# Optimization experiments

Measured on AMD Instinct MI355X. Metric: run time of the kernel, lower is better.

The kernel has to match this reference:

```python
import jax, jax.numpy as jnp
import numpy as np

D_MODEL = 1024
D_INNER = 2048   # d_model * expansion_factor(2)
D_CONV = 4
N_EXPERTS = 8
TOP_K = 2


def setup_inputs() -> dict:
    key = jax.random.key(0)
    ks = jax.random.split(key, 6)
    s = 0.02
    return {
        "x": jax.random.normal(ks[0], (4, 2048, D_MODEL), jnp.float32),
        "Wr": jax.random.normal(ks[1], (N_EXPERTS, D_MODEL), jnp.float32) * s,
        "br": jnp.zeros((N_EXPERTS,), jnp.float32),
        "Win": jax.random.normal(ks[2], (N_EXPERTS, 2 * D_INNER, D_MODEL), jnp.float32) * s,
        "conv_w": jax.random.normal(ks[3], (N_EXPERTS, D_INNER, D_CONV), jnp.float32) * s,
        "conv_b": jnp.zeros((N_EXPERTS, D_INNER), jnp.float32),
        "Dp": jnp.ones((N_EXPERTS, D_INNER), jnp.float32),
        "Wout": jax.random.normal(ks[4], (N_EXPERTS, D_MODEL, D_INNER), jnp.float32) * s,
    }


def reference(x, Wr, br, Win, conv_w, conv_b, Dp, Wout):
    B, L, C = x.shape
    xf = x.reshape(-1, C)                                   # [N, C]
    logits = xf @ Wr.T + br                                 # [N, E]
    probs = jax.nn.softmax(logits.astype(jnp.float32), axis=-1)
    tw, ti = jax.lax.top_k(probs, TOP_K)                    # [N, k]
    tw = tw / jnp.sum(tw, axis=-1, keepdims=True)
    oh = jax.nn.one_hot(ti, N_EXPERTS, dtype=jnp.float32)   # [N, k, E]
    load = oh.sum(1).mean(0)                                # [E]
    aux_loss = jnp.sum(load * load)
    # per-token combine weight for each expert (sum over top-k slots)
    cw = jnp.einsum('nk,nke->ne', tw, oh)                   # [N, E]
    out = jnp.zeros_like(xf)
    for j in range(N_EXPERTS):
        # Per-token expert (L=1 inside the original loop): causal depthwise
        # conv with left padding reduces to last-tap * x + bias.
        xz = xf @ Win[j].T                                  # [N, 2*D_INNER]
        xi, z = xz[:, :D_INNER], xz[:, D_INNER:]
        xa = jax.nn.silu(xi * conv_w[j, :, -1] + conv_b[j])
        y = xa * Dp[j] * jax.nn.silu(z)
        out = out + cw[:, j:j + 1].astype(xf.dtype) * (y @ Wout[j].T)
    return out.reshape(B, L, C), aux_loss
```

## Files before the change

kernel.cpp:

```cpp
#include <hip/hip_runtime.h>
#include <hip/hip_bf16.h>
#include <stdint.h>

#define NTOK 8192
#define CDIM 1024
#define DIN  2048
#define NEXP 8
#define NSLOT (NTOK * 2)

typedef __bf16 bf16x8 __attribute__((ext_vector_type(8)));
typedef float  f32x4  __attribute__((ext_vector_type(4)));

typedef __attribute__((address_space(1))) const unsigned char GBUF;
typedef __attribute__((address_space(3))) unsigned char LBUF;

__device__ __forceinline__ void gload_lds16(const void* g, void* l) {
    __builtin_amdgcn_global_load_lds((GBUF*)g, (LBUF*)l, 16, 0, 0);
}

__device__ __forceinline__ ushort f2bf(float f) {
    union { float f; unsigned u; } v; v.f = f;
    unsigned u = v.u;
    u += 0x7fffu + ((u >> 16) & 1u);
    return (ushort)(u >> 16);
}
__device__ __forceinline__ float bf2f(ushort u) {
    union { float f; unsigned u; } v; v.u = ((unsigned)u) << 16; return v.f;
}
__device__ __forceinline__ float silu_f(float x) { return x / (1.f + __expf(-x)); }

__device__ __forceinline__ bf16x8 lds_swz(const ushort* L, int row, int kof) {
    return *(const bf16x8*)&L[row * 64 + ((((kof >> 3) ^ row) & 7) << 3)];
}

__global__ void __launch_bounds__(256) k_cvt(const float* __restrict__ src,
                                             ushort* __restrict__ dst, int n4) {
    int i = blockIdx.x * 256 + threadIdx.x;
    int stride = gridDim.x * 256;
    for (; i < n4; i += stride) {
        float4 v = ((const float4*)src)[i];
        ushort4 o;
        o.x = f2bf(v.x); o.y = f2bf(v.y); o.z = f2bf(v.z); o.w = f2bf(v.w);
        ((ushort4*)dst)[i] = o;
    }
}

__global__ void __launch_bounds__(256) k_router(
    const float* __restrict__ x, const float* __restrict__ Wr,
    const float* __restrict__ br, int* __restrict__ counts,
    int* __restrict__ tok_e, float* __restrict__ tok_w,
    ushort* __restrict__ xb) {
    int wave = blockIdx.x * 4 + (threadIdx.x >> 6);
    int lane = threadIdx.x & 63;
    const float4* row = (const float4*)(x + (size_t)wave * CDIM);
    ushort4* xrow = (ushort4*)(xb + (size_t)wave * CDIM);
    float acc[NEXP];
#pragma unroll
    for (int e = 0; e < NEXP; ++e) acc[e] = 0.f;
#pragma unroll
    for (int j = 0; j < 4; ++j) {
        float4 v = row[j * 64 + lane];
        ushort4 o;
        o.x = f2bf(v.x); o.y = f2bf(v.y); o.z = f2bf(v.z); o.w = f2bf(v.w);
        xrow[j * 64 + lane] = o;
#pragma unroll
        for (int e = 0; e < NEXP; ++e) {
            float4 w = ((const float4*)(Wr + e * CDIM))[j * 64 + lane];
            acc[e] += v.x * w.x + v.y * w.y + v.z * w.z + v.w * w.w;
        }
    }
#pragma unroll
    for (int off = 32; off > 0; off >>= 1)
#pragma unroll
        for (int e = 0; e < NEXP; ++e) acc[e] += __shfl_xor(acc[e], off, 64);
    if (lane == 0) {
        float l[NEXP];
#pragma unroll
        for (int e = 0; e < NEXP; ++e) l[e] = acc[e] + br[e];
        int i0 = 0; float l0 = l[0];
#pragma unroll
        for (int e = 1; e < NEXP; ++e) if (l[e] > l0) { l0 = l[e]; i0 = e; }
        int i1 = -1; float l1 = -1e30f;
#pragma unroll
        for (int e = 0; e < NEXP; ++e) if (e != i0 && l[e] > l1) { l1 = l[e]; i1 = e; }
        float s  = __expf(l1 - l0);
        float w0 = 1.f / (1.f + s);
        float w1 = 1.f - w0;
        tok_e[wave * 2] = i0; tok_e[wave * 2 + 1] = i1;
        tok_w[wave * 2] = w0; tok_w[wave * 2 + 1] = w1;
        atomicAdd(&counts[i0], 1); atomicAdd(&counts[i1], 1);
    }
}

__global__ void k_scan(const int* __restrict__ counts, int* __restrict__ offsets,
                       float* __restrict__ out_aux) {
    if (threadIdx.x == 0 && blockIdx.x == 0) {
        int o = 0;
        for (int e = 0; e < NEXP; ++e) { offsets[e] = o; o += counts[e]; }
        offsets[NEXP] = o;
        float aux = 0.f;
        for (int e = 0; e < NEXP; ++e) {
            float ld = (float)counts[e] * (1.f / (float)NTOK);
            aux += ld * ld;
        }
        *out_aux = aux;
    }
}

__global__ void __launch_bounds__(256) k_scatter(
    const int* __restrict__ tok_e, const float* __restrict__ tok_w,
    const int* __restrict__ offsets, int* __restrict__ cursor,
    int* __restrict__ perm_token, int* __restrict__ tok_slot) {
    int t = blockIdx.x * 256 + threadIdx.x;
    if (t >= NTOK) return;
#pragma unroll
    for (int k = 0; k < 2; ++k) {
        int e = tok_e[t * 2 + k];
        int pos = atomicAdd(&cursor[e], 1);
        int s = offsets[e] + pos;
        perm_token[s] = t;
        tok_slot[t * 2 + k] = s;
    }
}

__global__ void __launch_bounds__(512, 2) k_gemm1(
    const ushort* __restrict__ xb, const ushort* __restrict__ Winb,
    const float* __restrict__ conv_w, const float* __restrict__ conv_b,
    const float* __restrict__ Dp, const int* __restrict__ counts,
    const int* __restrict__ offsets, const int* __restrict__ perm_token,
    ushort* __restrict__ y) {
    int h = blockIdx.x;
    int vb = (h & 7) * 160 + (h >> 3);
    int e   = vb / 160;
    int r   = vb % 160;
    int mt0 = r >> 4;
    int nt  = r & 15;
    int cnt = counts[e];
    if (cnt == 0) return;
    int base = offsets[e];
    int mtiles = (cnt + 255) >> 8;
    int n0 = nt * 128;

    __shared__ ushort aL[2][256 * 64];
    __shared__ ushort bL[2][256 * 64];

    int tid = threadIdx.x, lane = tid & 63, w = tid >> 6;
    int Mw = w >> 1, Nw = w & 1;
    const ushort* WinE = Winb + (size_t)e * (2 * DIN) * CDIM;
    int schunk = ((tid & 7) ^ ((tid >> 3) & 7)) << 3;

    uint bsrc[4];
#pragma unroll
    for (int i = 0; i < 4; ++i) {
        int rr = i * 64 + (tid >> 3);
        int grow = (rr < 128) ? (n0 + rr) : (DIN + n0 + (rr - 128));
        bsrc[i] = (uint)grow * CDIM + schunk;
    }

#define STAGE1(bi, kk0) do { \
        gload_lds16(xb   + asrc[0] + (kk0), &aL[bi][(0 * 512 + tid) * 8]); \
        gload_lds16(xb   + asrc[1] + (kk0), &aL[bi][(1 * 512 + tid) * 8]); \
        gload_lds16(xb   + asrc[2] + (kk0), &aL[bi][(2 * 512 + tid) * 8]); \
        gload_lds16(xb   + asrc[3] + (kk0), &aL[bi][(3 * 512 + tid) * 8]); \
        gload_lds16(WinE + bsrc[0] + (kk0), &bL[bi][(0 * 512 + tid) * 8]); \
        gload_lds16(WinE + bsrc[1] + (kk0), &bL[bi][(1 * 512 + tid) * 8]); \
        gload_lds16(WinE + bsrc[2] + (kk0), &bL[bi][(2 * 512 + tid) * 8]); \
        gload_lds16(WinE + bsrc[3] + (kk0), &bL[bi][(3 * 512 + tid) * 8]); \
    } while (0)

    for (int mt = mt0; mt < mtiles; mt += 10) {
        int rem = cnt - mt * 256;
        uint asrc[4];
#pragma unroll
        for (int i = 0; i < 4; ++i) {
            int rr = i * 64 + (tid >> 3);
            int sidx = base + mt * 256 + (rr < rem ? rr : 0);
            asrc[i] = (uint)perm_token[sidx] * CDIM + schunk;
        }

        f32x4 accXi[4][4], accZ[4][4];
#pragma unroll
        for (int m = 0; m < 4; ++m)
#pragma unroll
            for (int n = 0; n < 4; ++n) {
                accXi[m][n] = f32x4{0.f, 0.f, 0.f, 0.f};
                accZ[m][n]  = f32x4{0.f, 0.f, 0.f, 0.f};
            }

        STAGE1(0, 0);
        __syncthreads();
#pragma unroll 2
        for (int kt = 0; kt < 16; ++kt) {
            int cur = kt & 1;
            if (kt < 15) STAGE1(cur ^ 1, (kt + 1) * 64);
            const ushort* A = &aL[cur][0];
            const ushort* B = &bL[cur][0];
#pragma unroll
            for (int kk = 0; kk < 64; kk += 32) {
                int kof = kk + (lane >> 4) * 8;
                bf16x8 af[4], bxi[4], bz[4];
#pragma unroll
                for (int m = 0; m < 4; ++m)
                    af[m] = lds_swz(A, Mw * 64 + m * 16 + (lane & 15), kof);
#pragma unroll
                for (int n = 0; n < 4; ++n) {
                    int cl = Nw * 64 + n * 16 + (lane & 15);
                    bxi[n] = lds_swz(B, cl, kof);
                    bz[n]  = lds_swz(B, 128 + cl, kof);
                }
#pragma unroll
                for (int m = 0; m < 4; ++m)
#pragma unroll
                    for (int n = 0; n < 4; ++n) {
                        accXi[m][n] = __builtin_amdgcn_mfma_f32_16x16x32_bf16(af[m], bxi[n], accXi[m][n], 0, 0, 0);
                        accZ[m][n]  = __builtin_amdgcn_mfma_f32_16x16x32_bf16(af[m], bz[n],  accZ[m][n],  0, 0, 0);
                    }
            }
            __syncthreads();
        }
#pragma unroll
        for (int n = 0; n < 4; ++n) {
            int c = n0 + Nw * 64 + n * 16 + (lane & 15);
            float cwl = conv_w[((size_t)e * DIN + c) * 4 + 3];
            float cb  = conv_b[(size_t)e * DIN + c];
            float dp  = Dp[(size_t)e * DIN + c];
#pragma unroll
            for (int m = 0; m < 4; ++m)
#pragma unroll
                for (int q = 0; q < 4; ++q) {
                    int rl = Mw * 64 + m * 16 + (lane >> 4) * 4 + q;
                    if (rl < rem) {
                        int slot = base + mt * 256 + rl;
                        float xi = accXi[m][n][q], z = accZ[m][n][q];
                        float yv = silu_f(xi * cwl + cb) * dp * silu_f(z);
                        y[(size_t)slot * DIN + c] = f2bf(yv);
                    }
                }
        }
    }
#undef STAGE1
}

__global__ void __launch_bounds__(512, 2) k_gemm2(
    const ushort* __restrict__ y, const ushort* __restrict__ Woutb,
    const int* __restrict__ counts, const int* __restrict__ offsets,
    ushort* __restrict__ so) {
    int h = blockIdx.x;
    int vb = (h & 7) * 32 + (h >> 3);
    int e   = vb >> 5;
    int r   = vb & 31;
    int nt  = r >> 3;
    int sp  = r & 7;
    int cnt = counts[e];
    if (cnt == 0) return;
    int base = offsets[e];
    int mtiles = (cnt + 255) >> 8;
    int c0 = nt * 256;

    __shared__ ushort aL[2][256 * 64];
    __shared__ ushort bL[2][256 * 64];

    int tid = threadIdx.x, lane = tid & 63, w = tid >> 6;
    int Mw = w >> 2, Nw = w & 3;
    const ushort* WoutE = Woutb + (size_t)e * CDIM * DIN;
    int schunk = ((tid & 7) ^ ((tid >> 3) & 7)) << 3;

    uint bsrc[4];
#pragma unroll
    for (int i = 0; i < 4; ++i) {
        int rr = i * 64 + (tid >> 3);
        bsrc[i] = (uint)(c0 + rr) * DIN + schunk;
    }

#define STAGE2(bi, kk0) do { \
        gload_lds16(y     + asrc[0] + (kk0), &aL[bi][(0 * 512 + tid) * 8]); \
        gload_lds16(y     + asrc[1] + (kk0), &aL[bi][(1 * 512 + tid) * 8]); \
        gload_lds16(y     + asrc[2] + (kk0), &aL[bi][(2 * 512 + tid) * 8]); \
        gload_lds16(y     + asrc[3] + (kk0), &aL[bi][(3 * 512 + tid) * 8]); \
        gload_lds16(WoutE + bsrc[0] + (kk0), &bL[bi][(0 * 512 + tid) * 8]); \
        gload_lds16(WoutE + bsrc[1] + (kk0), &bL[bi][(1 * 512 + tid) * 8]); \
        gload_lds16(WoutE + bsrc[2] + (kk0), &bL[bi][(2 * 512 + tid) * 8]); \
        gload_lds16(WoutE + bsrc[3] + (kk0), &bL[bi][(3 * 512 + tid) * 8]); \
    } while (0)

    for (int mt = sp; mt < mtiles; mt += 8) {
        int rem = cnt - mt * 256;
        uint asrc[4];
#pragma unroll
        for (int i = 0; i < 4; ++i) {
            int rr = i * 64 + (tid >> 3);
            int slot = base + mt * 256 + (rr < rem ? rr : 0);
            asrc[i] = (uint)slot * DIN + schunk;
        }
        f32x4 acc[8][4];
#pragma unroll
        for (int m = 0; m < 8; ++m)
#pragma unroll
            for (int n = 0; n < 4; ++n) acc[m][n] = f32x4{0.f, 0.f, 0.f, 0.f};

        STAGE2(0, 0);
        __syncthreads();
#pragma unroll 2
        for (int kt = 0; kt < 32; ++kt) {
            int cur = kt & 1;
            if (kt < 31) STAGE2(cur ^ 1, (kt + 1) * 64);
            const ushort* A = &aL[cur][0];
            const ushort* B = &bL[cur][0];
#pragma unroll
            for (int kk = 0; kk < 64; kk += 32) {
                int kof = kk + (lane >> 4) * 8;
                bf16x8 af[8], bfr[4];
#pragma unroll
                for (int m = 0; m < 8; ++m)
                    af[m] = lds_swz(A, Mw * 128 + m * 16 + (lane & 15), kof);
#pragma unroll
                for (int n = 0; n < 4; ++n)
                    bfr[n] = lds_swz(B, Nw * 64 + n * 16 + (lane & 15), kof);
#pragma unroll
                for (int m = 0; m < 8; ++m)
#pragma unroll
                    for (int n = 0; n < 4; ++n)
                        acc[m][n] = __builtin_amdgcn_mfma_f32_16x16x32_bf16(af[m], bfr[n], acc[m][n], 0, 0, 0);
            }
            __syncthreads();
        }
#pragma unroll
        for (int m = 0; m < 8; ++m)
#pragma unroll
            for (int q = 0; q < 4; ++q) {
                int rl = Mw * 128 + m * 16 + (lane >> 4) * 4 + q;
                if (rl < rem) {
                    int slot = base + mt * 256 + rl;
#pragma unroll
                    for (int n = 0; n < 4; ++n) {
                        int col = c0 + Nw * 64 + n * 16 + (lane & 15);
                        so[(size_t)slot * CDIM + col] = f2bf(acc[m][n][q]);
                    }
                }
            }
    }
#undef STAGE2
}

__global__ void __launch_bounds__(256) k_combine(
    const ushort* __restrict__ so, const int* __restrict__ tok_slot,
    const float* __restrict__ tok_w, float* __restrict__ out) {
    int i = blockIdx.x * 256 + threadIdx.x;
    int t  = i >> 7;
    int c8 = (i & 127) << 3;
    int s0 = tok_slot[t * 2], s1 = tok_slot[t * 2 + 1];
    float w0 = tok_w[t * 2],  w1 = tok_w[t * 2 + 1];
    uint4 a = *(const uint4*)(so + (size_t)s0 * CDIM + c8);
    uint4 b = *(const uint4*)(so + (size_t)s1 * CDIM + c8);
    const ushort* au = (const ushort*)&a;
    const ushort* bu = (const ushort*)&b;
    float4 o0, o1;
    o0.x = w0 * bf2f(au[0]) + w1 * bf2f(bu[0]);
    o0.y = w0 * bf2f(au[1]) + w1 * bf2f(bu[1]);
    o0.z = w0 * bf2f(au[2]) + w1 * bf2f(bu[2]);
    o0.w = w0 * bf2f(au[3]) + w1 * bf2f(bu[3]);
    o1.x = w0 * bf2f(au[4]) + w1 * bf2f(bu[4]);
    o1.y = w0 * bf2f(au[5]) + w1 * bf2f(bu[5]);
    o1.z = w0 * bf2f(au[6]) + w1 * bf2f(bu[6]);
    o1.w = w0 * bf2f(au[7]) + w1 * bf2f(bu[7]);
    float4* dst = (float4*)(out + (size_t)t * CDIM + c8);
    dst[0] = o0; dst[1] = o1;
}

extern "C" void kernel_launch(void* const* d_in, const int* in_sizes, int n_in,
                              void* d_out, int out_size, void* d_ws, size_t ws_size,
                              hipStream_t stream) {
    const float* x      = (const float*)d_in[0];
    const float* Wr     = (const float*)d_in[1];
    const float* br     = (const float*)d_in[2];
    const float* Win    = (const float*)d_in[3];
    const float* conv_w = (const float*)d_in[4];
    const float* conv_b = (const float*)d_in[5];
    const float* Dp     = (const float*)d_in[6];
    const float* Wout   = (const float*)d_in[7];
    float* out = (float*)d_out;

    char* ws = (char*)d_ws;
    int*    counts     = (int*)(ws + 0);
    int*    offsets    = (int*)(ws + 64);
    int*    cursor     = (int*)(ws + 128);
    int*    tok_e      = (int*)(ws + 4096);
    float*  tok_w      = (float*)(ws + 4096 + 1 * 65536);
    int*    perm_token = (int*)(ws + 4096 + 2 * 65536);
    int*    tok_slot   = (int*)(ws + 4096 + 3 * 65536);
    const size_t MB = 1u << 20;
    ushort* y     = (ushort*)(ws + MB);
    ushort* xb    = (ushort*)(ws + MB + 67108864);
    ushort* winb  = (ushort*)(ws + MB + 67108864 + 16777216);
    ushort* woutb = (ushort*)(ws + MB + 67108864 + 16777216 + 67108864);
    ushort* so    = winb;

    hipMemsetAsync(ws, 0, 256, stream);

    k_cvt<<<2048, 256, 0, stream>>>(Win,  winb,  NEXP * 2 * DIN * CDIM / 4);
    k_cvt<<<1024, 256, 0, stream>>>(Wout, woutb, NEXP * CDIM * DIN / 4);

    k_router<<<NTOK / 4, 256, 0, stream>>>(x, Wr, br, counts, tok_e, tok_w, xb);
    k_scan<<<1, 64, 0, stream>>>(counts, offsets, out + (size_t)NTOK * CDIM);
    k_scatter<<<NTOK / 256, 256, 0, stream>>>(tok_e, tok_w, offsets, cursor, perm_token, tok_slot);

    k_gemm1<<<NEXP * 160, 512, 0, stream>>>(xb, winb, conv_w, conv_b, Dp,
                                            counts, offsets, perm_token, y);
    k_gemm2<<<NEXP * 32, 512, 0, stream>>>(y, woutb, counts, offsets, so);
    k_combine<<<NTOK * 128 / 256, 256, 0, stream>>>(so, tok_slot, tok_w, out);
}
```

Measured before the change: 632.2 us.

## Use 4-stage K=32 LDS pipeline with vmcnt waits in both expert GEMMs

Replaces the double-buffered K=64 tiles with a four-slot ring of K=32 tiles in both expert GEMMs. Each step waits on outstanding global-to-LDS loads with explicit s_waitcnt vmcnt and a bare s_barrier instead of __syncthreads, so three tiles stay in flight. The MFMA sections are wrapped in s_setprio, and the XOR swizzle is dropped for a plain 32-wide row layout. The aim is to hide global load latency better; the cost is possible LDS bank conflicts from the unswizzled 64-byte rows and more barriers per unit of K.

```diff
diff --git a/kernel.cpp b/kernel.cpp
--- a/kernel.cpp
+++ b/kernel.cpp
@@ -29,9 +29,8 @@
 }
 __device__ __forceinline__ float silu_f(float x) { return x / (1.f + __expf(-x)); }
 
-__device__ __forceinline__ bf16x8 lds_swz(const ushort* L, int row, int kof) {
-    return *(const bf16x8*)&L[row * 64 + ((((kof >> 3) ^ row) & 7) << 3)];
-}
+#define WAITV(N) asm volatile("s_waitcnt vmcnt(" #N ")" ::: "memory")
+#define BARR     __builtin_amdgcn_s_barrier()
 
 __global__ void __launch_bounds__(256) k_cvt(const float* __restrict__ src,
                                              ushort* __restrict__ dst, int n4) {
@@ -141,42 +140,24 @@
     int mtiles = (cnt + 255) >> 8;
     int n0 = nt * 128;
 
-    __shared__ ushort aL[2][256 * 64];
-    __shared__ ushort bL[2][256 * 64];
+    __shared__ ushort aL[4][256 * 32];
+    __shared__ ushort bL[4][256 * 32];
 
     int tid = threadIdx.x, lane = tid & 63, w = tid >> 6;
     int Mw = w >> 1, Nw = w & 1;
     const ushort* WinE = Winb + (size_t)e * (2 * DIN) * CDIM;
-    int schunk = ((tid & 7) ^ ((tid >> 3) & 7)) << 3;
-
-    uint bsrc[4];
-#pragma unroll
-    for (int i = 0; i < 4; ++i) {
-        int rr = i * 64 + (tid >> 3);
-        int grow = (rr < 128) ? (n0 + rr) : (DIN + n0 + (rr - 128));
-        bsrc[i] = (uint)grow * CDIM + schunk;
-    }
-
-#define STAGE1(bi, kk0) do { \
-        gload_lds16(xb   + asrc[0] + (kk0), &aL[bi][(0 * 512 + tid) * 8]); \
-        gload_lds16(xb   + asrc[1] + (kk0), &aL[bi][(1 * 512 + tid) * 8]); \
-        gload_lds16(xb   + asrc[2] + (kk0), &aL[bi][(2 * 512 + tid) * 8]); \
-        gload_lds16(xb   + asrc[3] + (kk0), &aL[bi][(3 * 512 + tid) * 8]); \
-        gload_lds16(WinE + bsrc[0] + (kk0), &bL[bi][(0 * 512 + tid) * 8]); \
-        gload_lds16(WinE + bsrc[1] + (kk0), &bL[bi][(1 * 512 + tid) * 8]); \
-        gload_lds16(WinE + bsrc[2] + (kk0), &bL[bi][(2 * 512 + tid) * 8]); \
-        gload_lds16(WinE + bsrc[3] + (kk0), &bL[bi][(3 * 512 + tid) * 8]); \
-    } while (0)
+
+    int srow0 = w * 16 + (lane >> 2);
+    int srow1 = srow0 + 128;
+    int skc   = (lane & 3) * 8;
+
+    uint b0 = (uint)(n0 + srow0) * CDIM + skc;
+    uint b1 = (uint)(DIN + n0 + (srow1 - 128)) * CDIM + skc;
 
     for (int mt = mt0; mt < mtiles; mt += 10) {
         int rem = cnt - mt * 256;
-        uint asrc[4];
-#pragma unroll
-        for (int i = 0; i < 4; ++i) {
-            int rr = i * 64 + (tid >> 3);
-            int sidx = base + mt * 256 + (rr < rem ? rr : 0);
-            asrc[i] = (uint)perm_token[sidx] * CDIM + schunk;
-        }
+        uint a0 = (uint)perm_token[base + mt * 256 + (srow0 < rem ? srow0 : 0)] * CDIM + skc;
+        uint a1 = (uint)perm_token[base + mt * 256 + (srow1 < rem ? srow1 : 0)] * CDIM + skc;
 
         f32x4 accXi[4][4], accZ[4][4];
 #pragma unroll
@@ -187,37 +168,52 @@
                 accZ[m][n]  = f32x4{0.f, 0.f, 0.f, 0.f};
             }
 
-        STAGE1(0, 0);
-        __syncthreads();
-#pragma unroll 2
-        for (int kt = 0; kt < 16; ++kt) {
-            int cur = kt & 1;
-            if (kt < 15) STAGE1(cur ^ 1, (kt + 1) * 64);
-            const ushort* A = &aL[cur][0];
-            const ushort* B = &bL[cur][0];
-#pragma unroll
-            for (int kk = 0; kk < 64; kk += 32) {
-                int kof = kk + (lane >> 4) * 8;
-                bf16x8 af[4], bxi[4], bz[4];
-#pragma unroll
-                for (int m = 0; m < 4; ++m)
-                    af[m] = lds_swz(A, Mw * 64 + m * 16 + (lane & 15), kof);
+        auto stage = [&](int slot, int c) {
+            int ko = c * 32;
+            gload_lds16(xb   + a0 + ko, &aL[slot][w * 512]);
+            gload_lds16(xb   + a1 + ko, &aL[slot][(w + 8) * 512]);
+            gload_lds16(WinE + b0 + ko, &bL[slot][w * 512]);
+            gload_lds16(WinE + b1 + ko, &bL[slot][(w + 8) * 512]);
+        };
+        auto compute = [&](int slot) {
+            const ushort* A = aL[slot];
+            const ushort* B = bL[slot];
+            int ko = (lane >> 4) * 8;
+            bf16x8 af[4], bxi[4], bz[4];
+#pragma unroll
+            for (int m = 0; m < 4; ++m)
+                af[m] = *(const bf16x8*)&A[(Mw * 64 + m * 16 + (lane & 15)) * 32 + ko];
+#pragma unroll
+            for (int n = 0; n < 4; ++n) {
+                int cl = Nw * 64 + n * 16 + (lane & 15);
+                bxi[n] = *(const bf16x8*)&B[cl * 32 + ko];
+                bz[n]  = *(const bf16x8*)&B[(128 + cl) * 32 + ko];
+            }
+            __builtin_amdgcn_s_setprio(1);
+#pragma unroll
+            for (int m = 0; m < 4; ++m)
 #pragma unroll
                 for (int n = 0; n < 4; ++n) {
-                    int cl = Nw * 64 + n * 16 + (lane & 15);
-                    bxi[n] = lds_swz(B, cl, kof);
-                    bz[n]  = lds_swz(B, 128 + cl, kof);
+                    accXi[m][n] = __builtin_amdgcn_mfma_f32_16x16x32_bf16(af[m], bxi[n], accXi[m][n], 0, 0, 0);
+                    accZ[m][n]  = __builtin_amdgcn_mfma_f32_16x16x32_bf16(af[m], bz[n],  accZ[m][n],  0, 0, 0);
                 }
-#pragma unroll
-                for (int m = 0; m < 4; ++m)
-#pragma unroll
-                    for (int n = 0; n < 4; ++n) {
-                        accXi[m][n] = __builtin_amdgcn_mfma_f32_16x16x32_bf16(af[m], bxi[n], accXi[m][n], 0, 0, 0);
-                        accZ[m][n]  = __builtin_amdgcn_mfma_f32_16x16x32_bf16(af[m], bz[n],  accZ[m][n],  0, 0, 0);
-                    }
-            }
-            __syncthreads();
+            __builtin_amdgcn_s_setprio(0);
+        };
+
+        stage(0, 0); stage(1, 1); stage(2, 2);
+#pragma unroll 1
+        for (int c = 0; c < 28; c += 4) {
+            WAITV(8); BARR; stage(3, c + 3); compute(0);
+            WAITV(8); BARR; stage(0, c + 4); compute(1);
+            WAITV(8); BARR; stage(1, c + 5); compute(2);
+            WAITV(8); BARR; stage(2, c + 6); compute(3);
         }
+        WAITV(8); BARR; stage(3, 31); compute(0);
+        WAITV(8); BARR; compute(1);
+        WAITV(4); BARR; compute(2);
+        WAITV(0); BARR; compute(3);
+        BARR;
+
 #pragma unroll
         for (int n = 0; n < 4; ++n) {
             int c = n0 + Nw * 64 + n * 16 + (lane & 15);
@@ -238,7 +234,6 @@
                 }
         }
     }
-#undef STAGE1
 }
 
 __global__ void __launch_bounds__(512, 2) k_gemm2(
@@ -257,73 +252,72 @@
     int mtiles = (cnt + 255) >> 8;
     int c0 = nt * 256;
 
-    __shared__ ushort aL[2][256 * 64];
-    __shared__ ushort bL[2][256 * 64];
+    __shared__ ushort aL[4][256 * 32];
+    __shared__ ushort bL[4][256 * 32];
 
     int tid = threadIdx.x, lane = tid & 63, w = tid >> 6;
     int Mw = w >> 2, Nw = w & 3;
     const ushort* WoutE = Woutb + (size_t)e * CDIM * DIN;
-    int schunk = ((tid & 7) ^ ((tid >> 3) & 7)) << 3;
-
-    uint bsrc[4];
-#pragma unroll
-    for (int i = 0; i < 4; ++i) {
-        int rr = i * 64 + (tid >> 3);
-        bsrc[i] = (uint)(c0 + rr) * DIN + schunk;
-    }
-
-#define STAGE2(bi, kk0) do { \
-        gload_lds16(y     + asrc[0] + (kk0), &aL[bi][(0 * 512 + tid) * 8]); \
-        gload_lds16(y     + asrc[1] + (kk0), &aL[bi][(1 * 512 + tid) * 8]); \
-        gload_lds16(y     + asrc[2] + (kk0), &aL[bi][(2 * 512 + tid) * 8]); \
-        gload_lds16(y     + asrc[3] + (kk0), &aL[bi][(3 * 512 + tid) * 8]); \
-        gload_lds16(WoutE + bsrc[0] + (kk0), &bL[bi][(0 * 512 + tid) * 8]); \
-        gload_lds16(WoutE + bsrc[1] + (kk0), &bL[bi][(1 * 512 + tid) * 8]); \
-        gload_lds16(WoutE + bsrc[2] + (kk0), &bL[bi][(2 * 512 + tid) * 8]); \
-        gload_lds16(WoutE + bsrc[3] + (kk0), &bL[bi][(3 * 512 + tid) * 8]); \
-    } while (0)
+
+    int srow0 = w * 16 + (lane >> 2);
+    int srow1 = srow0 + 128;
+    int skc   = (lane & 3) * 8;
+
+    uint b0 = (uint)(c0 + srow0) * DIN + skc;
+    uint b1 = (uint)(c0 + srow1) * DIN + skc;
 
     for (int mt = sp; mt < mtiles; mt += 8) {
         int rem = cnt - mt * 256;
-        uint asrc[4];
-#pragma unroll
-        for (int i = 0; i < 4; ++i) {
-            int rr = i * 64 + (tid >> 3);
-            int slot = base + mt * 256 + (rr < rem ? rr : 0);
-            asrc[i] = (uint)slot * DIN + schunk;
+        uint a0 = (uint)(base + mt * 256 + (srow0 < rem ? srow0 : 0)) * DIN + skc;
+        uint a1 = (uint)(base + mt * 256 + (srow1 < rem ? srow1 : 0)) * DIN + skc;
+
+        f32x4 acc[8][4];
+#pragma unroll
+        for (int m = 0; m < 8; ++m)
+#pragma unroll
+            for (int n = 0; n < 4; ++n) acc[m][n] = f32x4{0.f, 0.f, 0.f, 0.f};
+
+        auto stage = [&](int slot, int c) {
+            int ko = c * 32;
+            gload_lds16(y     + a0 + ko, &aL[slot][w * 512]);
+            gload_lds16(y     + a1 + ko, &aL[slot][(w + 8) * 512]);
+            gload_lds16(WoutE + b0 + ko, &bL[slot][w * 512]);
+            gload_lds16(WoutE + b1 + ko, &bL[slot][(w + 8) * 512]);
+        };
+        auto compute = [&](int slot) {
+            const ushort* A = aL[slot];
+            const ushort* B = bL[slot];
+            int ko = (lane >> 4) * 8;
+            bf16x8 af[8], bfr[4];
+#pragma unroll
+            for (int m = 0; m < 8; ++m)
+                af[m] = *(const bf16x8*)&A[(Mw * 128 + m * 16 + (lane & 15)) * 32 + ko];
+#pragma unroll
+            for (int n = 0; n < 4; ++n)
+                bfr[n] = *(const bf16x8*)&B[(Nw * 64 + n * 16 + (lane & 15)) * 32 + ko];
+            __builtin_amdgcn_s_setprio(1);
+#pragma unroll
+            for (int m = 0; m < 8; ++m)
+#pragma unroll
+                for (int n = 0; n < 4; ++n)
+                    acc[m][n] = __builtin_amdgcn_mfma_f32_16x16x32_bf16(af[m], bfr[n], acc[m][n], 0, 0, 0);
+            __builtin_amdgcn_s_setprio(0);
+        };
+
+        stage(0, 0); stage(1, 1); stage(2, 2);
+#pragma unroll 1
+        for (int c = 0; c < 60; c += 4) {
+            WAITV(8); BARR; stage(3, c + 3); compute(0);
+            WAITV(8); BARR; stage(0, c + 4); compute(1);
+            WAITV(8); BARR; stage(1, c + 5); compute(2);
+            WAITV(8); BARR; stage(2, c + 6); compute(3);
         }
-        f32x4 acc[8][4];
-#pragma unroll
-        for (int m = 0; m < 8; ++m)
-#pragma unroll
-            for (int n = 0; n < 4; ++n) acc[m][n] = f32x4{0.f, 0.f, 0.f, 0.f};
-
-        STAGE2(0, 0);
-        __syncthreads();
-#pragma unroll 2
-        for (int kt = 0; kt < 32; ++kt) {
-            int cur = kt & 1;
-            if (kt < 31) STAGE2(cur ^ 1, (kt + 1) * 64);
-            const ushort* A = &aL[cur][0];
-            const ushort* B = &bL[cur][0];
-#pragma unroll
-            for (int kk = 0; kk < 64; kk += 32) {
-                int kof = kk + (lane >> 4) * 8;
-                bf16x8 af[8], bfr[4];
-#pragma unroll
-                for (int m = 0; m < 8; ++m)
-                    af[m] = lds_swz(A, Mw * 128 + m * 16 + (lane & 15), kof);
-#pragma unroll
-                for (int n = 0; n < 4; ++n)
-                    bfr[n] = lds_swz(B, Nw * 64 + n * 16 + (lane & 15), kof);
-#pragma unroll
-                for (int m = 0; m < 8; ++m)
-#pragma unroll
-                    for (int n = 0; n < 4; ++n)
-                        acc[m][n] = __builtin_amdgcn_mfma_f32_16x16x32_bf16(af[m], bfr[n], acc[m][n], 0, 0, 0);
-            }
-            __syncthreads();
-        }
+        WAITV(8); BARR; stage(3, 63); compute(0);
+        WAITV(8); BARR; compute(1);
+        WAITV(4); BARR; compute(2);
+        WAITV(0); BARR; compute(3);
+        BARR;
+
 #pragma unroll
         for (int m = 0; m < 8; ++m)
 #pragma unroll
@@ -339,7 +333,6 @@
                 }
             }
     }
-#undef STAGE2
 }
 
 __global__ void __launch_bounds__(256) k_combine(
```

After: 694.8 us. 1.1x slower.

## Interleave split prefetch with MFMA phases and raise wave priority in both GEMMs

Applied to the files above, without the earlier changes.

The k-loop of both expert GEMM kernels becomes four phases per k-tile. Each phase loads a subset of fragments from LDS, issues a quarter of the next tile's global-to-LDS copies, then runs its MFMA block with wave priority raised. Explicit vmcnt waits and raw barriers replace whole-tile staging plus __syncthreads, so copies overlap compute more finely and stalls shrink. The cost is more barriers per tile, fragile hand-counted waitcnt ordering, and loops no longer unrolled.

```diff
diff --git a/kernel.cpp b/kernel.cpp
--- a/kernel.cpp
+++ b/kernel.cpp
@@ -32,6 +32,9 @@
 __device__ __forceinline__ bf16x8 lds_swz(const ushort* L, int row, int kof) {
     return *(const bf16x8*)&L[row * 64 + ((((kof >> 3) ^ row) & 7) << 3)];
 }
+
+#define WAITV(N) asm volatile("s_waitcnt vmcnt(" #N ")" ::: "memory")
+#define BARR     __builtin_amdgcn_s_barrier()
 
 __global__ void __launch_bounds__(256) k_cvt(const float* __restrict__ src,
                                              ushort* __restrict__ dst, int n4) {
@@ -157,17 +160,6 @@
         bsrc[i] = (uint)grow * CDIM + schunk;
     }
 
-#define STAGE1(bi, kk0) do { \
-        gload_lds16(xb   + asrc[0] + (kk0), &aL[bi][(0 * 512 + tid) * 8]); \
-        gload_lds16(xb   + asrc[1] + (kk0), &aL[bi][(1 * 512 + tid) * 8]); \
-        gload_lds16(xb   + asrc[2] + (kk0), &aL[bi][(2 * 512 + tid) * 8]); \
-        gload_lds16(xb   + asrc[3] + (kk0), &aL[bi][(3 * 512 + tid) * 8]); \
-        gload_lds16(WinE + bsrc[0] + (kk0), &bL[bi][(0 * 512 + tid) * 8]); \
-        gload_lds16(WinE + bsrc[1] + (kk0), &bL[bi][(1 * 512 + tid) * 8]); \
-        gload_lds16(WinE + bsrc[2] + (kk0), &bL[bi][(2 * 512 + tid) * 8]); \
-        gload_lds16(WinE + bsrc[3] + (kk0), &bL[bi][(3 * 512 + tid) * 8]); \
-    } while (0)
-
     for (int mt = mt0; mt < mtiles; mt += 10) {
         int rem = cnt - mt * 256;
         uint asrc[4];
@@ -187,37 +179,84 @@
                 accZ[m][n]  = f32x4{0.f, 0.f, 0.f, 0.f};
             }
 
-        STAGE1(0, 0);
+        auto stgA = [&](int bi, int ko, int i, int j) {
+            gload_lds16(xb + asrc[i] + ko, &aL[bi][(i * 512 + tid) * 8]);
+            gload_lds16(xb + asrc[j] + ko, &aL[bi][(j * 512 + tid) * 8]);
+        };
+        auto stgB = [&](int bi, int ko, int i, int j) {
+            gload_lds16(WinE + bsrc[i] + ko, &bL[bi][(i * 512 + tid) * 8]);
+            gload_lds16(WinE + bsrc[j] + ko, &bL[bi][(j * 512 + tid) * 8]);
+        };
+
+        bf16x8 af0[4], af1[4], bx[4], bz[4];
+        stgA(0, 0, 0, 1); stgA(0, 0, 2, 3); stgB(0, 0, 0, 1); stgB(0, 0, 2, 3);
+
+#pragma unroll 1
+        for (int kt = 0; kt < 16; ++kt) {
+            int cur = kt & 1, nxt = cur ^ 1;
+            const ushort* A = aL[cur];
+            const ushort* B = bL[cur];
+            int ko = (kt + 1) * 64;
+            bool st = kt < 15;
+            WAITV(2);
+            BARR;
+#pragma unroll
+            for (int m = 0; m < 4; ++m)
+                af0[m] = lds_swz(A, Mw * 64 + m * 16 + (lane & 15), (lane >> 4) * 8);
+#pragma unroll
+            for (int n = 0; n < 4; ++n)
+                bx[n] = lds_swz(B, Nw * 64 + n * 16 + (lane & 15), (lane >> 4) * 8);
+            if (st) stgA(nxt, ko, 0, 1);
+            __builtin_amdgcn_s_setprio(1);
+#pragma unroll
+            for (int m = 0; m < 4; ++m)
+#pragma unroll
+                for (int n = 0; n < 4; ++n)
+                    accXi[m][n] = __builtin_amdgcn_mfma_f32_16x16x32_bf16(af0[m], bx[n], accXi[m][n], 0, 0, 0);
+            __builtin_amdgcn_s_setprio(0);
+            if (st) { WAITV(2); } else { WAITV(0); }
+            BARR;
+#pragma unroll
+            for (int n = 0; n < 4; ++n)
+                bz[n] = lds_swz(B, 128 + Nw * 64 + n * 16 + (lane & 15), (lane >> 4) * 8);
+            if (st) stgA(nxt, ko, 2, 3);
+            __builtin_amdgcn_s_setprio(1);
+#pragma unroll
+            for (int m = 0; m < 4; ++m)
+#pragma unroll
+                for (int n = 0; n < 4; ++n)
+                    accZ[m][n] = __builtin_amdgcn_mfma_f32_16x16x32_bf16(af0[m], bz[n], accZ[m][n], 0, 0, 0);
+            __builtin_amdgcn_s_setprio(0);
+            BARR;
+#pragma unroll
+            for (int m = 0; m < 4; ++m)
+                af1[m] = lds_swz(A, Mw * 64 + m * 16 + (lane & 15), 32 + (lane >> 4) * 8);
+#pragma unroll
+            for (int n = 0; n < 4; ++n)
+                bx[n] = lds_swz(B, Nw * 64 + n * 16 + (lane & 15), 32 + (lane >> 4) * 8);
+            if (st) stgB(nxt, ko, 0, 1);
+            __builtin_amdgcn_s_setprio(1);
+#pragma unroll
+            for (int m = 0; m < 4; ++m)
+#pragma unroll
+                for (int n = 0; n < 4; ++n)
+                    accXi[m][n] = __builtin_amdgcn_mfma_f32_16x16x32_bf16(af1[m], bx[n], accXi[m][n], 0, 0, 0);
+            __builtin_amdgcn_s_setprio(0);
+            BARR;
+#pragma unroll
+            for (int n = 0; n < 4; ++n)
+                bz[n] = lds_swz(B, 128 + Nw * 64 + n * 16 + (lane & 15), 32 + (lane >> 4) * 8);
+            if (st) stgB(nxt, ko, 2, 3);
+            __builtin_amdgcn_s_setprio(1);
+#pragma unroll
+            for (int m = 0; m < 4; ++m)
+#pragma unroll
+                for (int n = 0; n < 4; ++n)
+                    accZ[m][n] = __builtin_amdgcn_mfma_f32_16x16x32_bf16(af1[m], bz[n], accZ[m][n], 0, 0, 0);
+            __builtin_amdgcn_s_setprio(0);
+        }
         __syncthreads();
-#pragma unroll 2
-        for (int kt = 0; kt < 16; ++kt) {
-            int cur = kt & 1;
-            if (kt < 15) STAGE1(cur ^ 1, (kt + 1) * 64);
-            const ushort* A = &aL[cur][0];
-            const ushort* B = &bL[cur][0];
-#pragma unroll
-            for (int kk = 0; kk < 64; kk += 32) {
-                int kof = kk + (lane >> 4) * 8;
-                bf16x8 af[4], bxi[4], bz[4];
-#pragma unroll
-                for (int m = 0; m < 4; ++m)
-                    af[m] = lds_swz(A, Mw * 64 + m * 16 + (lane & 15), kof);
-#pragma unroll
-                for (int n = 0; n < 4; ++n) {
-                    int cl = Nw * 64 + n * 16 + (lane & 15);
-                    bxi[n] = lds_swz(B, cl, kof);
-                    bz[n]  = lds_swz(B, 128 + cl, kof);
-                }
-#pragma unroll
-                for (int m = 0; m < 4; ++m)
-#pragma unroll
-                    for (int n = 0; n < 4; ++n) {
-                        accXi[m][n] = __builtin_amdgcn_mfma_f32_16x16x32_bf16(af[m], bxi[n], accXi[m][n], 0, 0, 0);
-                        accZ[m][n]  = __builtin_amdgcn_mfma_f32_16x16x32_bf16(af[m], bz[n],  accZ[m][n],  0, 0, 0);
-                    }
-            }
-            __syncthreads();
-        }
+
 #pragma unroll
         for (int n = 0; n < 4; ++n) {
             int c = n0 + Nw * 64 + n * 16 + (lane & 15);
@@ -237,8 +276,8 @@
                     }
                 }
         }
-    }
-#undef STAGE1
+        __syncthreads();
+    }
 }
 
 __global__ void __launch_bounds__(512, 2) k_gemm2(
@@ -272,17 +311,6 @@
         bsrc[i] = (uint)(c0 + rr) * DIN + schunk;
     }
 
-#define STAGE2(bi, kk0) do { \
-        gload_lds16(y     + asrc[0] + (kk0), &aL[bi][(0 * 512 + tid) * 8]); \
-        gload_lds16(y     + asrc[1] + (kk0), &aL[bi][(1 * 512 + tid) * 8]); \
-        gload_lds16(y     + asrc[2] + (kk0), &aL[bi][(2 * 512 + tid) * 8]); \
-        gload_lds16(y     + asrc[3] + (kk0), &aL[bi][(3 * 512 + tid) * 8]); \
-        gload_lds16(WoutE + bsrc[0] + (kk0), &bL[bi][(0 * 512 + tid) * 8]); \
-        gload_lds16(WoutE + bsrc[1] + (kk0), &bL[bi][(1 * 512 + tid) * 8]); \
-        gload_lds16(WoutE + bsrc[2] + (kk0), &bL[bi][(2 * 512 + tid) * 8]); \
-        gload_lds16(WoutE + bsrc[3] + (kk0), &bL[bi][(3 * 512 + tid) * 8]); \
-    } while (0)
-
     for (int mt = sp; mt < mtiles; mt += 8) {
         int rem = cnt - mt * 256;
         uint asrc[4];
@@ -298,32 +326,83 @@
 #pragma unroll
             for (int n = 0; n < 4; ++n) acc[m][n] = f32x4{0.f, 0.f, 0.f, 0.f};
 
-        STAGE2(0, 0);
+        auto stgA = [&](int bi, int ko, int i, int j) {
+            gload_lds16(y + asrc[i] + ko, &aL[bi][(i * 512 + tid) * 8]);
+            gload_lds16(y + asrc[j] + ko, &aL[bi][(j * 512 + tid) * 8]);
+        };
+        auto stgB = [&](int bi, int ko, int i, int j) {
+            gload_lds16(WoutE + bsrc[i] + ko, &bL[bi][(i * 512 + tid) * 8]);
+            gload_lds16(WoutE + bsrc[j] + ko, &bL[bi][(j * 512 + tid) * 8]);
+        };
+
+        bf16x8 afA[4], afB[4], bf0[4], bf1[4];
+        stgA(0, 0, 0, 1); stgA(0, 0, 2, 3); stgB(0, 0, 0, 1); stgB(0, 0, 2, 3);
+
+#pragma unroll 1
+        for (int kt = 0; kt < 32; ++kt) {
+            int cur = kt & 1, nxt = cur ^ 1;
+            const ushort* A = aL[cur];
+            const ushort* B = bL[cur];
+            int ko = (kt + 1) * 64;
+            bool st = kt < 31;
+            WAITV(0);
+            BARR;
+#pragma unroll
+            for (int m = 0; m < 4; ++m)
+                afA[m] = lds_swz(A, Mw * 128 + m * 16 + (lane & 15), (lane >> 4) * 8);
+#pragma unroll
+            for (int n = 0; n < 4; ++n)
+                bf0[n] = lds_swz(B, Nw * 64 + n * 16 + (lane & 15), (lane >> 4) * 8);
+            if (st) stgA(nxt, ko, 0, 1);
+            __builtin_amdgcn_s_setprio(1);
+#pragma unroll
+            for (int m = 0; m < 4; ++m)
+#pragma unroll
+                for (int n = 0; n < 4; ++n)
+                    acc[m][n] = __builtin_amdgcn_mfma_f32_16x16x32_bf16(afA[m], bf0[n], acc[m][n], 0, 0, 0);
+            __builtin_amdgcn_s_setprio(0);
+            BARR;
+#pragma unroll
+            for (int m = 0; m < 4; ++m)
+                afB[m] = lds_swz(A, Mw * 128 + 64 + m * 16 + (lane & 15), (lane >> 4) * 8);
+            if (st) stgA(nxt, ko, 2, 3);
+            __builtin_amdgcn_s_setprio(1);
+#pragma unroll
+            for (int m = 0; m < 4; ++m)
+#pragma unroll
+                for (int n = 0; n < 4; ++n)
+                    acc[4 + m][n] = __builtin_amdgcn_mfma_f32_16x16x32_bf16(afB[m], bf0[n], acc[4 + m][n], 0, 0, 0);
+            __builtin_amdgcn_s_setprio(0);
+            BARR;
+#pragma unroll
+            for (int m = 0; m < 4; ++m)
+                afA[m] = lds_swz(A, Mw * 128 + m * 16 + (lane & 15), 32 + (lane >> 4) * 8);
+#pragma unroll
+            for (int n = 0; n < 4; ++n)
+                bf1[n] = lds_swz(B, Nw * 64 + n * 16 + (lane & 15), 32 + (lane >> 4) * 8);
+            if (st) stgB(nxt, ko, 0, 1);
+            __builtin_amdgcn_s_setprio(1);
+#pragma unroll
+            for (int m = 0; m < 4; ++m)
+#pragma unroll
+                for (int n = 0; n < 4; ++n)
+                    acc[m][n] = __builtin_amdgcn_mfma_f32_16x16x32_bf16(afA[m], bf1[n], acc[m][n], 0, 0, 0);
+            __builtin_amdgcn_s_setprio(0);
+            BARR;
+#pragma unroll
+            for (int m = 0; m < 4; ++m)
+                afB[m] = lds_swz(A, Mw * 128 + 64 + m * 16 + (lane & 15), 32 + (lane >> 4) * 8);
+            if (st) stgB(nxt, ko, 2, 3);
+            __builtin_amdgcn_s_setprio(1);
+#pragma unroll
+            for (int m = 0; m < 4; ++m)
+#pragma unroll
+                for (int n = 0; n < 4; ++n)
+                    acc[4 + m][n] = __builtin_amdgcn_mfma_f32_16x16x32_bf16(afB[m], bf1[n], acc[4 + m][n], 0, 0, 0);
+            __builtin_amdgcn_s_setprio(0);
+        }
         __syncthreads();
-#pragma unroll 2
-        for (int kt = 0; kt < 32; ++kt) {
-            int cur = kt & 1;
-            if (kt < 31) STAGE2(cur ^ 1, (kt + 1) * 64);
-            const ushort* A = &aL[cur][0];
-            const ushort* B = &bL[cur][0];
-#pragma unroll
-            for (int kk = 0; kk < 64; kk += 32) {
-                int kof = kk + (lane >> 4) * 8;
-                bf16x8 af[8], bfr[4];
-#pragma unroll
-                for (int m = 0; m < 8; ++m)
-                    af[m] = lds_swz(A, Mw * 128 + m * 16 + (lane & 15), kof);
-#pragma unroll
-                for (int n = 0; n < 4; ++n)
-                    bfr[n] = lds_swz(B, Nw * 64 + n * 16 + (lane & 15), kof);
-#pragma unroll
-                for (int m = 0; m < 8; ++m)
-#pragma unroll
-                    for (int n = 0; n < 4; ++n)
-                        acc[m][n] = __builtin_amdgcn_mfma_f32_16x16x32_bf16(af[m], bfr[n], acc[m][n], 0, 0, 0);
-            }
-            __syncthreads();
-        }
+
 #pragma unroll
         for (int m = 0; m < 8; ++m)
 #pragma unroll
@@ -338,8 +417,8 @@
                     }
                 }
             }
-    }
-#undef STAGE2
+        __syncthreads();
+    }
 }
 
 __global__ void __launch_bounds__(256) k_combine(
```

New measurement: 626.3 us. About the same (-0.9%).
